# Kernel tuning notes

Measured on AMD Instinct MI355X. Metric: run time of the kernel, lower is better.

Reference implementation:

```python
import jax, jax.numpy as jnp
import numpy as np
from jax import lax

B, L, DM = 1, 2048, 1024   # batch, seq len, d_model
N = 16                     # d_state
K = 4                      # d_conv
DI = 2 * DM                # d_inner = d_model * expand_factor


def silu(v):
    return v * jax.nn.sigmoid(v)


def setup_inputs() -> dict:
    key = jax.random.key(0)
    ks = jax.random.split(key, 11)
    s = 0.02
    f32 = jnp.float32
    return {
        "x": jax.random.normal(ks[0], (B, L, DM), f32),
        "W_in": jax.random.normal(ks[1], (2 * DI, DM), f32) * s,
        "b_in": jnp.zeros((2 * DI,), f32),
        "W_conv": jax.random.normal(ks[2], (DI, 1, K), f32) * s,  # depthwise conv kernel (torch layout)
        "b_conv": jnp.zeros((DI,), f32),
        "W_x": jax.random.normal(ks[3], (DI + 2 * N, DI), f32) * s,
        "b_x": jnp.zeros((DI + 2 * N,), f32),
        "W_out": jax.random.normal(ks[4], (DM, DI), f32) * s,
        "b_out": jnp.zeros((DM,), f32),
        "A_log": jax.random.normal(ks[5], (DI, N), f32),
        "D": jnp.ones((DI,), f32),
    }


def reference(x, W_in, b_in, W_conv, b_conv, W_x, b_x, W_out, b_out, A_log, D):
    Bsz = x.shape[0]
    # in_proj and split into ssm branch / residual gate branch
    xr = x @ W_in.T + b_in                      # (B, L, 2*DI)
    xi, res = jnp.split(xr, 2, axis=-1)
    # causal depthwise conv1d: torch pads (K-1) both sides then slices [:L] == left-pad K-1
    xc = jnp.transpose(xi, (0, 2, 1))           # (B, DI, L)
    xc = lax.conv_general_dilated(
        xc, W_conv, window_strides=(1,), padding=[(K - 1, 0)],
        dimension_numbers=("NCH", "OIH", "NCH"), feature_group_count=DI,
    ) + b_conv[None, :, None]
    xi = silu(jnp.transpose(xc, (0, 2, 1)))     # (B, L, DI)
    # selective-scan parameterization
    proj = xi @ W_x.T + b_x                      # (B, L, DI + 2N)
    delta = jax.nn.softplus(proj[..., :DI])      # (B, L, DI)
    B_ssm = proj[..., DI:DI + N]                 # (B, L, N)
    C_ssm = proj[..., DI + N:]                   # (B, L, N)
    A = -jnp.exp(A_log)                          # (DI, N)
    dA = jnp.exp(delta[..., None] * A)                               # (B, L, DI, N)
    dBx = delta[..., None] * B_ssm[:, :, None, :] * xi[..., None]    # (B, L, DI, N)

    def step(h, inp):
        da, dbx, c = inp
        h = da * h + dbx                         # (B, DI, N)
        y = jnp.einsum("bdn,bn->bd", h, c)
        return h, y

    h0 = jnp.zeros((Bsz, DI, N), x.dtype)
    _, ys = lax.scan(
        step, h0,
        (jnp.swapaxes(dA, 0, 1), jnp.swapaxes(dBx, 0, 1), jnp.swapaxes(C_ssm, 0, 1)),
    )
    y = jnp.swapaxes(ys, 0, 1) + xi * D          # skip connection
    y = y * silu(res)                            # gate
    return y @ W_out.T + b_out                   # (B, L, DM)
```

## Files before the change

### kernel.cpp

```cpp
#include <hip/hip_runtime.h>
#include <stdint.h>

#define L_SEQ 2048
#define DMODEL 1024
#define DI_DIM 2048
#define NSSM 16
#define NPROJ 2080
#define NCHUNK 64
#define LCHUNK 32

typedef __attribute__((ext_vector_type(8))) short bf16x8;
typedef __attribute__((ext_vector_type(4))) float f32x4;

__device__ __forceinline__ float bf2f(unsigned short u) {
  union { uint32_t u; float f; } v; v.u = (uint32_t)u << 16; return v.f;
}
__device__ __forceinline__ unsigned short f2bf(float f) {
  union { float f; uint32_t u; } v; v.f = f;
  uint32_t u = v.u;
  return (unsigned short)((u + 0x7fffu + ((u >> 16) & 1u)) >> 16);
}
__device__ __forceinline__ void async16(const void* g, void* l) {
  __builtin_amdgcn_global_load_lds(
      (__attribute__((address_space(1))) void*)(g),
      (__attribute__((address_space(3))) void*)(l), 16, 0, 0);
}
__device__ __forceinline__ float softplusf(float p) {
  return (p > 20.f) ? p : __logf(1.f + __expf(p));
}
__device__ __forceinline__ float siluf(float x) {
  return x * __builtin_amdgcn_rcpf(1.f + __expf(-x));
}

#define WAITV(N) asm volatile("s_waitcnt vmcnt(" #N ")" ::: "memory")
#define GBAR()                                   \
  {                                              \
    __builtin_amdgcn_s_barrier();                \
    asm volatile("" ::: "memory");               \
  }

#define CVT_N1 524288
#define CVT_N2 (CVT_N1 + 1048576)
#define CVT_N3 (CVT_N2 + 1064960)
__global__ void k_convert3(const float* __restrict__ x, const float* __restrict__ win,
                           const float* __restrict__ wx, unsigned short* __restrict__ xb,
                           unsigned short* __restrict__ winb, unsigned short* __restrict__ wxb) {
  int i = blockIdx.x * 256 + threadIdx.x;
  const float4* src; unsigned short* dst; int j;
  if (i < CVT_N1)      { src = (const float4*)x;   dst = xb;   j = i; }
  else if (i < CVT_N2) { src = (const float4*)win; dst = winb; j = i - CVT_N1; }
  else if (i < CVT_N3) { src = (const float4*)wx;  dst = wxb;  j = i - CVT_N2; }
  else return;
  float4 v = src[j];
  ushort4 o;
  o.x = f2bf(v.x); o.y = f2bf(v.y); o.z = f2bf(v.z); o.w = f2bf(v.w);
  ((ushort4*)dst)[j] = o;
}

__global__ void k_f32_to_bf16(const float* __restrict__ in,
                              unsigned short* __restrict__ out, int n4) {
  int i = blockIdx.x * blockDim.x + threadIdx.x;
  if (i < n4) {
    const float4 v = ((const float4*)in)[i];
    ushort4 o;
    o.x = f2bf(v.x); o.y = f2bf(v.y); o.z = f2bf(v.z); o.w = f2bf(v.w);
    ((ushort4*)out)[i] = o;
  }
}

template <typename OutT, int DEPTH>
__global__ __launch_bounds__(256) void k_gemm_bt(
    const unsigned short* __restrict__ A, const unsigned short* __restrict__ B,
    const float* __restrict__ bias, OutT* __restrict__ C,
    int M, int N, int K) {
  __shared__ unsigned short As[DEPTH][64 * 32];
  __shared__ unsigned short Bs[DEPTH][128 * 32];
  const int tid = threadIdx.x;
  const int wave = tid >> 6;
  const int lane = tid & 63;
  const int m0 = blockIdx.y * 64;
  const int n0 = blockIdx.x * 128;
  const int kLen = K / gridDim.z;
  const int kLo = blockIdx.z * kLen;

  const int srow = lane >> 2;
  const int scol = ((lane & 3) ^ ((lane >> 3) & 3)) * 8;
  int ar = m0 + wave * 16 + srow;         if (ar > M - 1) ar = M - 1;
  int br0 = n0 + wave * 32 + srow;        if (br0 > N - 1) br0 = N - 1;
  int br1 = n0 + wave * 32 + 16 + srow;   if (br1 > N - 1) br1 = N - 1;
  const unsigned short* ap  = A + (size_t)ar * K + scol + kLo;
  const unsigned short* bp0 = B + (size_t)br0 * K + scol + kLo;
  const unsigned short* bp1 = B + (size_t)br1 * K + scol + kLo;
  const int soA  = wave * 512;
  const int soB0 = (wave * 2) * 512;
  const int soB1 = (wave * 2 + 1) * 512;

  const int mrow = lane & 15;
  const int swz8 = (((lane >> 4) ^ ((mrow >> 1) & 3)) * 8);
  const int ro = mrow * 32 + swz8;

  f32x4 acc[4][2];
#pragma unroll
  for (int i = 0; i < 4; i++)
#pragma unroll
    for (int j = 0; j < 2; j++) acc[i][j] = (f32x4){0.f, 0.f, 0.f, 0.f};

  const int niter = kLen / 32;

#define STAGE(BUF, KT)                                                         \
  {                                                                            \
    async16(ap + (KT), &As[BUF][soA]);                                         \
    async16(bp0 + (KT), &Bs[BUF][soB0]);                                       \
    async16(bp1 + (KT), &Bs[BUF][soB1]);                                       \
  }

#define GEMM_COMPUTE(BUF)                                                      \
  {                                                                            \
    bf16x8 af[4], bfv[2];                                                      \
    _Pragma("unroll")                                                          \
    for (int i = 0; i < 4; i++)                                                \
      af[i] = *(const bf16x8*)&As[BUF][i * 512 + ro];                          \
    _Pragma("unroll")                                                          \
    for (int j = 0; j < 2; j++)                                                \
      bfv[j] = *(const bf16x8*)&Bs[BUF][(wave * 2 + j) * 512 + ro];            \
    _Pragma("unroll")                                                          \
    for (int i = 0; i < 4; i++)                                                \
      _Pragma("unroll")                                                        \
      for (int j = 0; j < 2; j++)                                              \
        acc[i][j] = __builtin_amdgcn_mfma_f32_16x16x32_bf16(af[i], bfv[j],     \
                                                        acc[i][j], 0, 0, 0);   \
  }

#pragma unroll
  for (int j = 0; j < DEPTH - 1; j++) STAGE(j, j * 32)

  int cur = 0, nxt = DEPTH - 1;
  for (int t = 0; t < niter - (DEPTH - 1); t++) {
    if constexpr (DEPTH == 4) { WAITV(6); } else { WAITV(3); }
    GBAR()
    STAGE(nxt, (t + DEPTH - 1) * 32)
    GEMM_COMPUTE(cur)
    cur = (cur == DEPTH - 1) ? 0 : cur + 1;
    nxt = (nxt == DEPTH - 1) ? 0 : nxt + 1;
  }
  if constexpr (DEPTH == 4) {
    WAITV(6); GBAR()
    GEMM_COMPUTE(cur) cur = (cur == 3) ? 0 : cur + 1;
    WAITV(3); GBAR()
    GEMM_COMPUTE(cur) cur = (cur == 3) ? 0 : cur + 1;
    WAITV(0); GBAR()
    GEMM_COMPUTE(cur)
  } else {
    WAITV(3); GBAR()
    GEMM_COMPUTE(cur) cur = (cur == DEPTH - 1) ? 0 : cur + 1;
    WAITV(0); GBAR()
    GEMM_COMPUTE(cur)
  }
#undef STAGE
#undef GEMM_COMPUTE

  const bool withBias = (gridDim.z == 1);
  OutT* Cz = C + (size_t)blockIdx.z * ((size_t)M * N);
#pragma unroll
  for (int j = 0; j < 2; j++) {
    int col = n0 + wave * 32 + j * 16 + (lane & 15);
    if (col < N) {
      float bv = withBias ? bias[col] : 0.f;
#pragma unroll
      for (int i = 0; i < 4; i++) {
        int rbase = m0 + i * 16 + (lane >> 4) * 4;
#pragma unroll
        for (int r = 0; r < 4; r++) {
          float v = acc[i][j][r] + bv;
          if constexpr (sizeof(OutT) == 2)
            Cz[(size_t)(rbase + r) * N + col] = (OutT)f2bf(v);
          else
            Cz[(size_t)(rbase + r) * N + col] = (OutT)v;
        }
      }
    }
  }
}

__global__ void k_reduce_out(const float* __restrict__ part, const float* __restrict__ bias,
                             float* __restrict__ out) {
  int i = blockIdx.x * 256 + threadIdx.x;
  float4 a = ((const float4*)part)[i];
  float4 b = ((const float4*)(part + (size_t)L_SEQ * DMODEL))[i];
  int col = (i * 4) & (DMODEL - 1);
  float4 bb = *(const float4*)&bias[col];
  float4 o;
  o.x = a.x + b.x + bb.x; o.y = a.y + b.y + bb.y;
  o.z = a.z + b.z + bb.z; o.w = a.w + b.w + bb.w;
  ((float4*)out)[i] = o;
}

__global__ void k_conv_silu(const unsigned short* __restrict__ xr,
                            const float* __restrict__ Wc,
                            const float* __restrict__ bc,
                            unsigned short* __restrict__ xcb) {
  int idx = blockIdx.x * blockDim.x + threadIdx.x;
  if (idx >= L_SEQ * DI_DIM) return;
  int t = idx >> 11;
  int d = idx & (DI_DIM - 1);
  float acc = bc[d];
  const float* wd = Wc + d * 4;
  if (t >= 3) acc += bf2f(xr[(size_t)(t - 3) * (2 * DI_DIM) + d]) * wd[0];
  if (t >= 2) acc += bf2f(xr[(size_t)(t - 2) * (2 * DI_DIM) + d]) * wd[1];
  if (t >= 1) acc += bf2f(xr[(size_t)(t - 1) * (2 * DI_DIM) + d]) * wd[2];
  acc += bf2f(xr[(size_t)t * (2 * DI_DIM) + d]) * wd[3];
  xcb[idx] = f2bf(siluf(acc));
}

__global__ __launch_bounds__(256) void k_scan_a(
    const float* __restrict__ proj, const unsigned short* __restrict__ xcb,
    const float* __restrict__ A_log,
    float* __restrict__ Sdelta, float* __restrict__ hstate) {
  __shared__ float Bsh[LCHUNK * NSSM];
  const int d = blockIdx.x * 256 + threadIdx.x;
  const int c = blockIdx.y;
  const int t0 = c * LCHUNK;
  for (int i = threadIdx.x; i < LCHUNK * NSSM; i += 256) {
    int t = i >> 4, n = i & 15;
    Bsh[i] = proj[(size_t)(t0 + t) * NPROJ + DI_DIM + n];
  }
  __syncthreads();
  float Ar[NSSM], h[NSSM];
#pragma unroll
  for (int n = 0; n < NSSM; n++) {
    Ar[n] = -__expf(A_log[d * NSSM + n]);
    h[n] = 0.f;
  }
  const float* pp = proj + (size_t)t0 * NPROJ + d;
  const unsigned short* xp = xcb + (size_t)t0 * DI_DIM + d;
  float p_nxt = pp[0];
  unsigned short x_nxt = xp[0];
  float sd = 0.f;
  for (int t = 0; t < LCHUNK; t++) {
    float p = p_nxt;
    unsigned short xu = x_nxt;
    if (t + 1 < LCHUNK) {
      p_nxt = pp[(size_t)(t + 1) * NPROJ];
      x_nxt = xp[(size_t)(t + 1) * DI_DIM];
    }
    float delta = softplusf(p);
    float dx = delta * bf2f(xu);
    sd += delta;
#pragma unroll
    for (int n = 0; n < NSSM; n++)
      h[n] = __expf(delta * Ar[n]) * h[n] + dx * Bsh[t * NSSM + n];
  }
  Sdelta[(size_t)c * DI_DIM + d] = sd;
#pragma unroll
  for (int n = 0; n < NSSM; n++)
    hstate[((size_t)c * DI_DIM + d) * NSSM + n] = h[n];
}

__global__ void k_scan_b(const float* __restrict__ A_log,
                         const float* __restrict__ Sdelta,
                         float* __restrict__ hstate) {
  int tid = blockIdx.x * 256 + threadIdx.x;
  int d = tid >> 4;
  float A = -__expf(A_log[tid]);
  float carry = 0.f;
  float v_nxt = hstate[tid];
  float s_nxt = Sdelta[d];
  for (int c = 0; c < NCHUNK; c++) {
    float v = v_nxt, s = s_nxt;
    if (c + 1 < NCHUNK) {
      v_nxt = hstate[(size_t)(c + 1) * DI_DIM * NSSM + tid];
      s_nxt = Sdelta[(size_t)(c + 1) * DI_DIM + d];
    }
    hstate[(size_t)c * DI_DIM * NSSM + tid] = carry;
    carry = __expf(A * s) * carry + v;
  }
}

__global__ __launch_bounds__(256) void k_scan_c(
    const float* __restrict__ proj, const unsigned short* __restrict__ xcb,
    const float* __restrict__ A_log, const float* __restrict__ h0,
    const float* __restrict__ Dvec, const unsigned short* __restrict__ xr,
    unsigned short* __restrict__ ybf) {
  __shared__ float Bsh[LCHUNK * NSSM];
  __shared__ float Csh[LCHUNK * NSSM];
  const int d = blockIdx.x * 256 + threadIdx.x;
  const int c = blockIdx.y;
  const int t0 = c * LCHUNK;
  for (int i = threadIdx.x; i < LCHUNK * NSSM; i += 256) {
    int t = i >> 4, n = i & 15;
    Bsh[i] = proj[(size_t)(t0 + t) * NPROJ + DI_DIM + n];
    Csh[i] = proj[(size_t)(t0 + t) * NPROJ + DI_DIM + NSSM + n];
  }
  __syncthreads();
  float Ar[NSSM], h[NSSM];
#pragma unroll
  for (int n = 0; n < NSSM; n++) {
    Ar[n] = -__expf(A_log[d * NSSM + n]);
    h[n] = h0[((size_t)c * DI_DIM + d) * NSSM + n];
  }
  float Dd = Dvec[d];
  const float* pp = proj + (size_t)t0 * NPROJ + d;
  const unsigned short* xp = xcb + (size_t)t0 * DI_DIM + d;
  const unsigned short* rp = xr + (size_t)t0 * (2 * DI_DIM) + DI_DIM + d;
  float p_nxt = pp[0];
  unsigned short x_nxt = xp[0];
  unsigned short r_nxt = rp[0];
  for (int t = 0; t < LCHUNK; t++) {
    float p = p_nxt;
    unsigned short xu = x_nxt, ru = r_nxt;
    if (t + 1 < LCHUNK) {
      p_nxt = pp[(size_t)(t + 1) * NPROJ];
      x_nxt = xp[(size_t)(t + 1) * DI_DIM];
      r_nxt = rp[(size_t)(t + 1) * (2 * DI_DIM)];
    }
    float delta = softplusf(p);
    float xi = bf2f(xu);
    float dx = delta * xi;
    float y = 0.f;
#pragma unroll
    for (int n = 0; n < NSSM; n++) {
      h[n] = __expf(delta * Ar[n]) * h[n] + dx * Bsh[t * NSSM + n];
      y += h[n] * Csh[t * NSSM + n];
    }
    y += xi * Dd;
    y *= siluf(bf2f(ru));
    ybf[(size_t)(t0 + t) * DI_DIM + d] = f2bf(y);
  }
}

extern "C" void kernel_launch(void* const* d_in, const int* in_sizes, int n_in,
                              void* d_out, int out_size, void* d_ws, size_t ws_size,
                              hipStream_t stream) {
  const float* x      = (const float*)d_in[0];
  const float* W_in   = (const float*)d_in[1];
  const float* b_in   = (const float*)d_in[2];
  const float* W_conv = (const float*)d_in[3];
  const float* b_conv = (const float*)d_in[4];
  const float* W_x    = (const float*)d_in[5];
  const float* b_x    = (const float*)d_in[6];
  const float* W_out  = (const float*)d_in[7];
  const float* b_out  = (const float*)d_in[8];
  const float* A_log  = (const float*)d_in[9];
  const float* Dv     = (const float*)d_in[10];
  float* out = (float*)d_out;

  char* ws = (char*)d_ws;
  size_t off = 0;
  auto alloc = [&](size_t bytes) { void* p = ws + off; off += (bytes + 255) & ~(size_t)255; return p; };
  unsigned short* win_bf = (unsigned short*)alloc((size_t)4096 * DMODEL * 2);
  unsigned short* wx_bf  = (unsigned short*)alloc((size_t)NPROJ * DI_DIM * 2);
  unsigned short* x_bf   = (unsigned short*)alloc((size_t)L_SEQ * DMODEL * 2);
  unsigned short* xr_bf  = (unsigned short*)alloc((size_t)L_SEQ * 2 * DI_DIM * 2);
  unsigned short* xcb    = (unsigned short*)alloc((size_t)L_SEQ * DI_DIM * 2);
  float* proj            = (float*)alloc((size_t)L_SEQ * NPROJ * 4);
  float* Sdelta          = (float*)alloc((size_t)NCHUNK * DI_DIM * 4);
  float* hstate          = (float*)alloc((size_t)NCHUNK * DI_DIM * NSSM * 4);
  if (off > ws_size) return;
  unsigned short* ybf     = win_bf;
  unsigned short* wout_bf = x_bf;
  float* part             = proj;

  k_convert3<<<CVT_N3 / 256, 256, 0, stream>>>(x, W_in, W_x, x_bf, win_bf, wx_bf);

  {
    dim3 g(4096 / 128, L_SEQ / 64);
    k_gemm_bt<unsigned short, 3><<<g, 256, 0, stream>>>(x_bf, win_bf, b_in, xr_bf, L_SEQ, 4096, DMODEL);
  }
  k_f32_to_bf16<<<(DMODEL * DI_DIM / 4) / 256, 256, 0, stream>>>(W_out, wout_bf, DMODEL * DI_DIM / 4);
  k_conv_silu<<<(L_SEQ * DI_DIM) / 256, 256, 0, stream>>>(xr_bf, W_conv, b_conv, xcb);
  {
    dim3 g((NPROJ + 127) / 128, L_SEQ / 64);
    k_gemm_bt<float, 4><<<g, 256, 0, stream>>>(xcb, wx_bf, b_x, proj, L_SEQ, NPROJ, DI_DIM);
  }
  {
    dim3 ga(DI_DIM / 256, NCHUNK);
    k_scan_a<<<ga, 256, 0, stream>>>(proj, xcb, A_log, Sdelta, hstate);
    k_scan_b<<<(DI_DIM * NSSM) / 256, 256, 0, stream>>>(A_log, Sdelta, hstate);
    k_scan_c<<<ga, 256, 0, stream>>>(proj, xcb, A_log, hstate, Dv, xr_bf, ybf);
  }
  {
    dim3 g(DMODEL / 128, L_SEQ / 64, 2);
    k_gemm_bt<float, 4><<<g, 256, 0, stream>>>(ybf, wout_bf, b_out, part, L_SEQ, DMODEL, DI_DIM);
    k_reduce_out<<<(L_SEQ * DMODEL / 4) / 256, 256, 0, stream>>>(part, b_out, out);
  }
}
```

Baseline: 278.1 us.

## Split-K the x_proj and out_proj GEMMs, fold partial sums into scan kernels

The x_proj GEMM is split along K into two partial-sum buffers when workspace allows, and the scan kernels add both partials plus the bias on the fly. The out_proj GEMM goes from split-K 2 to split-K 4, with the fourth partial written into the reused xcb buffer and a four-way reduce kernel. Pipeline depth drops from 4 to 3 stages. The conv kernel is vectorised to 8 channels per thread, and the scan kernels use float4 hstate I/O and batched loads in scan_b. The aim is more blocks to fill the GPU on the skinny GEMMs, at the cost of extra partial-buffer traffic and redundant loads in the scans.

```diff
diff --git a/kernel.cpp b/kernel.cpp
--- a/kernel.cpp
+++ b/kernel.cpp
@@ -10,6 +10,7 @@
 #define LCHUNK 32
 
 typedef __attribute__((ext_vector_type(8))) short bf16x8;
+typedef __attribute__((ext_vector_type(8))) unsigned short u16x8;
 typedef __attribute__((ext_vector_type(4))) float f32x4;
 
 __device__ __forceinline__ float bf2f(unsigned short u) {
@@ -72,6 +73,7 @@
 __global__ __launch_bounds__(256) void k_gemm_bt(
     const unsigned short* __restrict__ A, const unsigned short* __restrict__ B,
     const float* __restrict__ bias, OutT* __restrict__ C,
+    OutT* __restrict__ Calt, int zAlt,
     int M, int N, int K) {
   __shared__ unsigned short As[DEPTH][64 * 32];
   __shared__ unsigned short Bs[DEPTH][128 * 32];
@@ -160,7 +162,9 @@
 #undef GEMM_COMPUTE
 
   const bool withBias = (gridDim.z == 1);
-  OutT* Cz = C + (size_t)blockIdx.z * ((size_t)M * N);
+  const int bz = blockIdx.z;
+  OutT* Cz = (bz < zAlt) ? (C + (size_t)bz * ((size_t)M * N))
+                         : (Calt + (size_t)(bz - zAlt) * ((size_t)M * N));
 #pragma unroll
   for (int j = 0; j < 2; j++) {
     int col = n0 + wave * 32 + j * 16 + (lane & 15);
@@ -182,16 +186,21 @@
   }
 }
 
-__global__ void k_reduce_out(const float* __restrict__ part, const float* __restrict__ bias,
-                             float* __restrict__ out) {
+__global__ void k_reduce_out4(const float* __restrict__ p, const float* __restrict__ pz3,
+                              const float* __restrict__ bias, float* __restrict__ out) {
   int i = blockIdx.x * 256 + threadIdx.x;
-  float4 a = ((const float4*)part)[i];
-  float4 b = ((const float4*)(part + (size_t)L_SEQ * DMODEL))[i];
+  const int N4 = L_SEQ * DMODEL / 4;
+  float4 a = ((const float4*)p)[i];
+  float4 b = ((const float4*)p)[i + N4];
+  float4 c = ((const float4*)p)[i + 2 * N4];
+  float4 d = ((const float4*)pz3)[i];
   int col = (i * 4) & (DMODEL - 1);
   float4 bb = *(const float4*)&bias[col];
   float4 o;
-  o.x = a.x + b.x + bb.x; o.y = a.y + b.y + bb.y;
-  o.z = a.z + b.z + bb.z; o.w = a.w + b.w + bb.w;
+  o.x = a.x + b.x + c.x + d.x + bb.x;
+  o.y = a.y + b.y + c.y + d.y + bb.y;
+  o.z = a.z + b.z + c.z + d.z + bb.z;
+  o.w = a.w + b.w + c.w + d.w + bb.w;
   ((float4*)out)[i] = o;
 }
 
@@ -199,30 +208,44 @@
                             const float* __restrict__ Wc,
                             const float* __restrict__ bc,
                             unsigned short* __restrict__ xcb) {
-  int idx = blockIdx.x * blockDim.x + threadIdx.x;
-  if (idx >= L_SEQ * DI_DIM) return;
-  int t = idx >> 11;
-  int d = idx & (DI_DIM - 1);
-  float acc = bc[d];
-  const float* wd = Wc + d * 4;
-  if (t >= 3) acc += bf2f(xr[(size_t)(t - 3) * (2 * DI_DIM) + d]) * wd[0];
-  if (t >= 2) acc += bf2f(xr[(size_t)(t - 2) * (2 * DI_DIM) + d]) * wd[1];
-  if (t >= 1) acc += bf2f(xr[(size_t)(t - 1) * (2 * DI_DIM) + d]) * wd[2];
-  acc += bf2f(xr[(size_t)t * (2 * DI_DIM) + d]) * wd[3];
-  xcb[idx] = f2bf(siluf(acc));
+  int idx = blockIdx.x * 256 + threadIdx.x;
+  int t = idx >> 8;
+  int d8 = (idx & 255) * 8;
+  const size_t rs = 2 * DI_DIM;
+  u16x8 x0 = (u16x8)(unsigned short)0, x1 = x0, x2 = x0;
+  u16x8 x3 = *(const u16x8*)&xr[(size_t)t * rs + d8];
+  if (t >= 1) x2 = *(const u16x8*)&xr[(size_t)(t - 1) * rs + d8];
+  if (t >= 2) x1 = *(const u16x8*)&xr[(size_t)(t - 2) * rs + d8];
+  if (t >= 3) x0 = *(const u16x8*)&xr[(size_t)(t - 3) * rs + d8];
+  float4 b0 = *(const float4*)&bc[d8];
+  float4 b1 = *(const float4*)&bc[d8 + 4];
+  float bb[8] = {b0.x, b0.y, b0.z, b0.w, b1.x, b1.y, b1.z, b1.w};
+  u16x8 o;
+#pragma unroll
+  for (int j = 0; j < 8; j++) {
+    float4 wd = *(const float4*)&Wc[(size_t)(d8 + j) * 4];
+    float acc = bb[j] + bf2f(x0[j]) * wd.x + bf2f(x1[j]) * wd.y +
+                bf2f(x2[j]) * wd.z + bf2f(x3[j]) * wd.w;
+    o[j] = f2bf(siluf(acc));
+  }
+  *(u16x8*)&xcb[(size_t)t * DI_DIM + d8] = o;
 }
 
 __global__ __launch_bounds__(256) void k_scan_a(
-    const float* __restrict__ proj, const unsigned short* __restrict__ xcb,
+    const float* __restrict__ p0, const float* __restrict__ p1f,
+    const float* __restrict__ bx, const unsigned short* __restrict__ xcb,
     const float* __restrict__ A_log,
     float* __restrict__ Sdelta, float* __restrict__ hstate) {
   __shared__ float Bsh[LCHUNK * NSSM];
   const int d = blockIdx.x * 256 + threadIdx.x;
   const int c = blockIdx.y;
   const int t0 = c * LCHUNK;
+  const float spf = (p1f != nullptr) ? 1.f : 0.f;
+  const float* p1 = (p1f != nullptr) ? p1f : p0;
   for (int i = threadIdx.x; i < LCHUNK * NSSM; i += 256) {
     int t = i >> 4, n = i & 15;
-    Bsh[i] = proj[(size_t)(t0 + t) * NPROJ + DI_DIM + n];
+    size_t o = (size_t)(t0 + t) * NPROJ + DI_DIM + n;
+    Bsh[i] = p0[o] + spf * (p1[o] + bx[DI_DIM + n]);
   }
   __syncthreads();
   float Ar[NSSM], h[NSSM];
@@ -231,19 +254,21 @@
     Ar[n] = -__expf(A_log[d * NSSM + n]);
     h[n] = 0.f;
   }
-  const float* pp = proj + (size_t)t0 * NPROJ + d;
+  const float bxd = spf * bx[d];
+  const float* pp = p0 + (size_t)t0 * NPROJ + d;
+  const float* pq = p1 + (size_t)t0 * NPROJ + d;
   const unsigned short* xp = xcb + (size_t)t0 * DI_DIM + d;
-  float p_nxt = pp[0];
+  float p_nxt = pp[0] + spf * pq[0];
   unsigned short x_nxt = xp[0];
   float sd = 0.f;
   for (int t = 0; t < LCHUNK; t++) {
     float p = p_nxt;
     unsigned short xu = x_nxt;
     if (t + 1 < LCHUNK) {
-      p_nxt = pp[(size_t)(t + 1) * NPROJ];
+      p_nxt = pp[(size_t)(t + 1) * NPROJ] + spf * pq[(size_t)(t + 1) * NPROJ];
       x_nxt = xp[(size_t)(t + 1) * DI_DIM];
     }
-    float delta = softplusf(p);
+    float delta = softplusf(p + bxd);
     float dx = delta * bf2f(xu);
     sd += delta;
 #pragma unroll
@@ -251,9 +276,11 @@
       h[n] = __expf(delta * Ar[n]) * h[n] + dx * Bsh[t * NSSM + n];
   }
   Sdelta[(size_t)c * DI_DIM + d] = sd;
-#pragma unroll
-  for (int n = 0; n < NSSM; n++)
-    hstate[((size_t)c * DI_DIM + d) * NSSM + n] = h[n];
+  float4* hp = (float4*)&hstate[((size_t)c * DI_DIM + d) * NSSM];
+  hp[0] = (float4){h[0], h[1], h[2], h[3]};
+  hp[1] = (float4){h[4], h[5], h[6], h[7]};
+  hp[2] = (float4){h[8], h[9], h[10], h[11]};
+  hp[3] = (float4){h[12], h[13], h[14], h[15]};
 }
 
 __global__ void k_scan_b(const float* __restrict__ A_log,
@@ -263,21 +290,24 @@
   int d = tid >> 4;
   float A = -__expf(A_log[tid]);
   float carry = 0.f;
-  float v_nxt = hstate[tid];
-  float s_nxt = Sdelta[d];
-  for (int c = 0; c < NCHUNK; c++) {
-    float v = v_nxt, s = s_nxt;
-    if (c + 1 < NCHUNK) {
-      v_nxt = hstate[(size_t)(c + 1) * DI_DIM * NSSM + tid];
-      s_nxt = Sdelta[(size_t)(c + 1) * DI_DIM + d];
-    }
-    hstate[(size_t)c * DI_DIM * NSSM + tid] = carry;
-    carry = __expf(A * s) * carry + v;
+  for (int cb = 0; cb < NCHUNK; cb += 8) {
+    float v[8], s[8];
+#pragma unroll
+    for (int j = 0; j < 8; j++) {
+      v[j] = hstate[(size_t)(cb + j) * DI_DIM * NSSM + tid];
+      s[j] = Sdelta[(size_t)(cb + j) * DI_DIM + d];
+    }
+#pragma unroll
+    for (int j = 0; j < 8; j++) {
+      hstate[(size_t)(cb + j) * DI_DIM * NSSM + tid] = carry;
+      carry = __expf(A * s[j]) * carry + v[j];
+    }
   }
 }
 
 __global__ __launch_bounds__(256) void k_scan_c(
-    const float* __restrict__ proj, const unsigned short* __restrict__ xcb,
+    const float* __restrict__ p0, const float* __restrict__ p1f,
+    const float* __restrict__ bx, const unsigned short* __restrict__ xcb,
     const float* __restrict__ A_log, const float* __restrict__ h0,
     const float* __restrict__ Dvec, const unsigned short* __restrict__ xr,
     unsigned short* __restrict__ ybf) {
@@ -286,34 +316,44 @@
   const int d = blockIdx.x * 256 + threadIdx.x;
   const int c = blockIdx.y;
   const int t0 = c * LCHUNK;
+  const float spf = (p1f != nullptr) ? 1.f : 0.f;
+  const float* p1 = (p1f != nullptr) ? p1f : p0;
   for (int i = threadIdx.x; i < LCHUNK * NSSM; i += 256) {
     int t = i >> 4, n = i & 15;
-    Bsh[i] = proj[(size_t)(t0 + t) * NPROJ + DI_DIM + n];
-    Csh[i] = proj[(size_t)(t0 + t) * NPROJ + DI_DIM + NSSM + n];
+    size_t ob = (size_t)(t0 + t) * NPROJ + DI_DIM + n;
+    size_t oc = ob + NSSM;
+    Bsh[i] = p0[ob] + spf * (p1[ob] + bx[DI_DIM + n]);
+    Csh[i] = p0[oc] + spf * (p1[oc] + bx[DI_DIM + NSSM + n]);
   }
   __syncthreads();
   float Ar[NSSM], h[NSSM];
 #pragma unroll
-  for (int n = 0; n < NSSM; n++) {
+  for (int n = 0; n < NSSM; n++)
     Ar[n] = -__expf(A_log[d * NSSM + n]);
-    h[n] = h0[((size_t)c * DI_DIM + d) * NSSM + n];
-  }
+  const float4* h0p = (const float4*)&h0[((size_t)c * DI_DIM + d) * NSSM];
+  float4 hv0 = h0p[0], hv1 = h0p[1], hv2 = h0p[2], hv3 = h0p[3];
+  h[0] = hv0.x; h[1] = hv0.y; h[2] = hv0.z; h[3] = hv0.w;
+  h[4] = hv1.x; h[5] = hv1.y; h[6] = hv1.z; h[7] = hv1.w;
+  h[8] = hv2.x; h[9] = hv2.y; h[10] = hv2.z; h[11] = hv2.w;
+  h[12] = hv3.x; h[13] = hv3.y; h[14] = hv3.z; h[15] = hv3.w;
   float Dd = Dvec[d];
-  const float* pp = proj + (size_t)t0 * NPROJ + d;
+  const float bxd = spf * bx[d];
+  const float* pp = p0 + (size_t)t0 * NPROJ + d;
+  const float* pq = p1 + (size_t)t0 * NPROJ + d;
   const unsigned short* xp = xcb + (size_t)t0 * DI_DIM + d;
   const unsigned short* rp = xr + (size_t)t0 * (2 * DI_DIM) + DI_DIM + d;
-  float p_nxt = pp[0];
+  float p_nxt = pp[0] + spf * pq[0];
   unsigned short x_nxt = xp[0];
   unsigned short r_nxt = rp[0];
   for (int t = 0; t < LCHUNK; t++) {
     float p = p_nxt;
     unsigned short xu = x_nxt, ru = r_nxt;
     if (t + 1 < LCHUNK) {
-      p_nxt = pp[(size_t)(t + 1) * NPROJ];
+      p_nxt = pp[(size_t)(t + 1) * NPROJ] + spf * pq[(size_t)(t + 1) * NPROJ];
       x_nxt = xp[(size_t)(t + 1) * DI_DIM];
       r_nxt = rp[(size_t)(t + 1) * (2 * DI_DIM)];
     }
-    float delta = softplusf(p);
+    float delta = softplusf(p + bxd);
     float xi = bf2f(xu);
     float dx = delta * xi;
     float y = 0.f;
@@ -356,31 +396,38 @@
   float* Sdelta          = (float*)alloc((size_t)NCHUNK * DI_DIM * 4);
   float* hstate          = (float*)alloc((size_t)NCHUNK * DI_DIM * NSSM * 4);
   if (off > ws_size) return;
+  float* part1 = nullptr;
+  {
+    size_t need = (size_t)L_SEQ * NPROJ * 4;
+    if (off + need <= ws_size) part1 = (float*)alloc(need);
+  }
   unsigned short* ybf     = win_bf;
   unsigned short* wout_bf = x_bf;
-  float* part             = proj;
 
   k_convert3<<<CVT_N3 / 256, 256, 0, stream>>>(x, W_in, W_x, x_bf, win_bf, wx_bf);
 
   {
     dim3 g(4096 / 128, L_SEQ / 64);
-    k_gemm_bt<unsigned short, 3><<<g, 256, 0, stream>>>(x_bf, win_bf, b_in, xr_bf, L_SEQ, 4096, DMODEL);
+    k_gemm_bt<unsigned short, 3><<<g, 256, 0, stream>>>(
+        x_bf, win_bf, b_in, xr_bf, (unsigned short*)nullptr, 8, L_SEQ, 4096, DMODEL);
   }
   k_f32_to_bf16<<<(DMODEL * DI_DIM / 4) / 256, 256, 0, stream>>>(W_out, wout_bf, DMODEL * DI_DIM / 4);
-  k_conv_silu<<<(L_SEQ * DI_DIM) / 256, 256, 0, stream>>>(xr_bf, W_conv, b_conv, xcb);
+  k_conv_silu<<<(L_SEQ * DI_DIM / 8) / 256, 256, 0, stream>>>(xr_bf, W_conv, b_conv, xcb);
   {
-    dim3 g((NPROJ + 127) / 128, L_SEQ / 64);
-    k_gemm_bt<float, 4><<<g, 256, 0, stream>>>(xcb, wx_bf, b_x, proj, L_SEQ, NPROJ, DI_DIM);
+    dim3 g((NPROJ + 127) / 128, L_SEQ / 64, part1 ? 2 : 1);
+    k_gemm_bt<float, 3><<<g, 256, 0, stream>>>(
+        xcb, wx_bf, b_x, proj, part1, 1, L_SEQ, NPROJ, DI_DIM);
   }
   {
     dim3 ga(DI_DIM / 256, NCHUNK);
-    k_scan_a<<<ga, 256, 0, stream>>>(proj, xcb, A_log, Sdelta, hstate);
+    k_scan_a<<<ga, 256, 0, stream>>>(proj, part1, b_x, xcb, A_log, Sdelta, hstate);
     k_scan_b<<<(DI_DIM * NSSM) / 256, 256, 0, stream>>>(A_log, Sdelta, hstate);
-    k_scan_c<<<ga, 256, 0, stream>>>(proj, xcb, A_log, hstate, Dv, xr_bf, ybf);
+    k_scan_c<<<ga, 256, 0, stream>>>(proj, part1, b_x, xcb, A_log, hstate, Dv, xr_bf, ybf);
   }
   {
-    dim3 g(DMODEL / 128, L_SEQ / 64, 2);
-    k_gemm_bt<float, 4><<<g, 256, 0, stream>>>(ybf, wout_bf, b_out, part, L_SEQ, DMODEL, DI_DIM);
-    k_reduce_out<<<(L_SEQ * DMODEL / 4) / 256, 256, 0, stream>>>(part, b_out, out);
-  }
-}
+    dim3 g(DMODEL / 128, L_SEQ / 64, 4);
+    k_gemm_bt<float, 3><<<g, 256, 0, stream>>>(
+        ybf, wout_bf, b_out, proj, (float*)xcb, 3, L_SEQ, DMODEL, DI_DIM);
+    k_reduce_out4<<<(L_SEQ * DMODEL / 4) / 256, 256, 0, stream>>>(proj, (float*)xcb, b_out, out);
+  }
+}
```

Result: no change. 279.6 us (+0.5%).
